# Optimization experiments

Measured on AMD Instinct MI355X. Metric: run time of the kernel, lower is better.

Reference implementation:

```python
import jax, jax.numpy as jnp
import numpy as np

N_HEAD = 16  # matches init_kwargs


def _rope_cos_sin(T, head_dim):
    # inv_freq over even indices, as in AdvancedRotaryEmbedding
    inv_freq = 1.0 / (10000.0 ** (jnp.arange(0, head_dim, 2, dtype=jnp.float32) / head_dim))
    t = jnp.arange(T, dtype=jnp.float32)
    freqs = t[:, None] * inv_freq[None, :]  # [T, head_dim/2]
    return jnp.cos(freqs), jnp.sin(freqs)


def _apply_rope(x, cos, sin):
    # x: [B, H, T, D]; cos/sin: [T, D/2] (broadcast over B, H)
    x1, x2 = x[..., 0::2], x[..., 1::2]
    # half-concat layout, faithful to the module's apply_rotary_emb
    return jnp.concatenate([x1 * cos - x2 * sin, x1 * sin + x2 * cos], axis=-1)


def reference(x, Wq, Wk, Wv, Wo):
    B, T, C = x.shape
    H = N_HEAD
    D = C // H
    # QKV projections (torch Linear: y = x @ W.T), then split heads -> [B, H, T, D]
    q = (x @ Wq.T).reshape(B, T, H, D).transpose(0, 2, 1, 3)
    k = (x @ Wk.T).reshape(B, T, H, D).transpose(0, 2, 1, 3)
    v = (x @ Wv.T).reshape(B, T, H, D).transpose(0, 2, 1, 3)
    cos, sin = _rope_cos_sin(T, D)
    cos = cos.astype(x.dtype)
    sin = sin.astype(x.dtype)
    q = _apply_rope(q, cos, sin)
    k = _apply_rope(k, cos, sin)
    # causal SDPA (eval mode -> dropout_p = 0); jax.nn expects [B, T, H, D]
    y = jax.nn.dot_product_attention(
        q.transpose(0, 2, 1, 3),
        k.transpose(0, 2, 1, 3),
        v.transpose(0, 2, 1, 3),
        is_causal=True,
    )  # [B, T, H, D]
    y = y.reshape(B, T, C)
    return y @ Wo.T


def setup_inputs() -> dict:
    key = jax.random.key(0)
    ks = jax.random.split(key, 5)
    B, T, C = 2, 2048, 1024
    s = 1.0 / np.sqrt(C)
    return {
        "x": jax.random.normal(ks[0], (B, T, C), dtype=jnp.float32),
        "Wq": jax.random.normal(ks[1], (C, C), dtype=jnp.float32) * s,
        "Wk": jax.random.normal(ks[2], (C, C), dtype=jnp.float32) * s,
        "Wv": jax.random.normal(ks[3], (C, C), dtype=jnp.float32) * s,
        "Wo": jax.random.normal(ks[4], (C, C), dtype=jnp.float32) * s,
    }
```

## Files before the change

### kernel.cpp

```cpp
#include <hip/hip_runtime.h>
#include <cstdint>
#include <cstddef>

typedef short s16x8 __attribute__((ext_vector_type(8)));
typedef float f32x4 __attribute__((ext_vector_type(4)));

#define MFMA16(a, b, c) __builtin_amdgcn_mfma_f32_16x16x32_bf16((a), (b), (c), 0, 0, 0)

constexpr int LDP = 72;
constexpr int LDW = 136;

__device__ __forceinline__ short f2bf(float f) {
    unsigned u = __builtin_bit_cast(unsigned, f);
    u += 0x7FFFu + ((u >> 16) & 1u);
    return (short)(u >> 16);
}
__device__ __forceinline__ float bf2f(short s) {
    unsigned u = ((unsigned)(unsigned short)s) << 16;
    return __builtin_bit_cast(float, u);
}
__device__ __forceinline__ unsigned pack2(float a, float b) {
    return (unsigned)(unsigned short)f2bf(a) | ((unsigned)(unsigned short)f2bf(b) << 16);
}
__device__ __forceinline__ unsigned pack2t(float a, float b) {
    unsigned ua = __builtin_bit_cast(unsigned, a);
    unsigned ub = __builtin_bit_cast(unsigned, b);
    return (ua >> 16) | (ub & 0xFFFF0000u);
}

__device__ __forceinline__ void async_ld16(const void* g, void* l) {
    __builtin_amdgcn_global_load_lds(
        (const __attribute__((address_space(1))) unsigned int*)g,
        (__attribute__((address_space(3))) unsigned int*)l, 16, 0, 0);
}

__global__ __launch_bounds__(256) void convert_kernel(
    const float* __restrict__ x, const float* __restrict__ Wq,
    const float* __restrict__ Wk, const float* __restrict__ Wv,
    const float* __restrict__ Wo, short* __restrict__ xb, short* __restrict__ wb) {
    const size_t f = ((size_t)blockIdx.x * 256 + threadIdx.x) * 8;
    const float* src;
    short* dst;
    if (f < 4194304) { src = x + f; dst = xb + f; }
    else {
        size_t wo = f - 4194304;
        int seg = (int)(wo >> 20);
        const float* ws4[4] = {Wq, Wk, Wv, Wo};
        src = ws4[seg] + (wo & 1048575u);
        dst = wb + wo;
    }
    float4 a = ((const float4*)src)[0];
    float4 b = ((const float4*)src)[1];
    *(uint4*)dst = make_uint4(pack2(a.x, a.y), pack2(a.z, a.w),
                              pack2(b.x, b.y), pack2(b.z, b.w));
}

__global__ __launch_bounds__(256) void qkv_kernel(
    const short* __restrict__ xb, const short* __restrict__ wb,
    short* __restrict__ Qo, short* __restrict__ Ko, short* __restrict__ VTo) {
    __shared__ __align__(16) short sA[128 * 64];
    __shared__ __align__(16) short sB[128 * 64];
    const int tid = threadIdx.x;
    const int w = tid >> 6, lane = tid & 63, quad = lane >> 4, l15 = lane & 15;
    const int wm = w & 1, wn = w >> 1;
    const int bx = blockIdx.x, by = blockIdx.y;
    const int m0 = by * 128;
    const int nb = bx * 128;

    f32x4 acc[4][4];
#pragma unroll
    for (int i = 0; i < 4; i++)
#pragma unroll
        for (int j = 0; j < 4; j++) acc[i][j] = f32x4{0.f, 0.f, 0.f, 0.f};

    for (int kb = 0; kb < 16; kb++) {
        const int k0 = kb * 64;
        if (kb) __syncthreads();
#pragma unroll
        for (int i = 0; i < 4; i++) {
            int c = i * 256 + tid;
            int row = c >> 3, col8 = (c & 7) * 8;
            async_ld16(xb + (size_t)(m0 + row) * 1024 + k0 + col8,
                       &sA[(i * 256 + w * 64) * 8]);
            async_ld16(wb + (size_t)(nb + row) * 1024 + k0 + col8,
                       &sB[(i * 256 + w * 64) * 8]);
        }
        __syncthreads();
#pragma unroll
        for (int ks = 0; ks < 2; ks++) {
            s16x8 av[4], bv[4];
#pragma unroll
            for (int at = 0; at < 4; at++)
                av[at] = *(const s16x8*)&sA[(wm * 64 + at * 16 + l15) * 64 + ks * 32 + quad * 8];
#pragma unroll
            for (int bt = 0; bt < 4; bt++)
                bv[bt] = *(const s16x8*)&sB[(wn * 64 + bt * 16 + l15) * 64 + ks * 32 + quad * 8];
#pragma unroll
            for (int at = 0; at < 4; at++)
#pragma unroll
                for (int bt = 0; bt < 4; bt++)
                    acc[at][bt] = MFMA16(av[at], bv[bt], acc[at][bt]);
        }
    }

    const int wsel = bx >> 3;
    const int h = (bx & 7) * 2 + wn;
    if (wsel == 2) {
#pragma unroll
        for (int at = 0; at < 4; at++) {
            int m = m0 + wm * 64 + at * 16 + quad * 4;
            int b = m >> 11, t0 = m & 2047;
            size_t base = ((size_t)((b * 16 + h) * 64)) * 2048;
#pragma unroll
            for (int bt = 0; bt < 4; bt++) {
                int d = bt * 16 + l15;
                unsigned lo = pack2(acc[at][bt][0], acc[at][bt][1]);
                unsigned hi = pack2(acc[at][bt][2], acc[at][bt][3]);
                *(uint2*)&VTo[base + (size_t)d * 2048 + t0] = make_uint2(lo, hi);
            }
        }
    } else {
        short* Out = (wsel == 0) ? Qo : Ko;
#pragma unroll
        for (int at = 0; at < 4; at++)
#pragma unroll
            for (int r = 0; r < 4; r++) {
                int m = m0 + wm * 64 + at * 16 + quad * 4 + r;
                int b = m >> 11, t = m & 2047;
                size_t base = (((size_t)(b * 16 + h)) * 2048 + t) * 64;
#pragma unroll
                for (int bt = 0; bt < 4; bt++)
                    Out[base + bt * 16 + l15] = f2bf(acc[at][bt][r]);
            }
    }
}

__global__ __launch_bounds__(256) void rope_kernel(short* __restrict__ Q, short* __restrict__ K) {
    const int rid = blockIdx.x * 256 + threadIdx.x;
    const bool isK = (rid & 65536) != 0;
    short* buf = isK ? K : Q;
    const float sc = isK ? 1.0f : 0.18033688011112042f;
    const int r2 = rid & 65535;
    const int t = r2 & 2047;
    short* row = buf + (size_t)r2 * 64;

    unsigned wv[32];
    const uint4* rp = (const uint4*)row;
#pragma unroll
    for (int c = 0; c < 8; c++) {
        uint4 v = rp[c];
        wv[c * 4 + 0] = v.x; wv[c * 4 + 1] = v.y; wv[c * 4 + 2] = v.z; wv[c * 4 + 3] = v.w;
    }
    float y1[32], y2[32];
    const float tf = (float)t;
#pragma unroll
    for (int i = 0; i < 32; i++) {
        float x1 = bf2f((short)(wv[i] & 0xFFFFu));
        float x2 = bf2f((short)(wv[i] >> 16));
        float inv = exp2f((float)i * -0.4152410118609203f);
        float rev = tf * inv * 0.15915494309189535f;
        rev = rev - floorf(rev);
        float sn = __builtin_amdgcn_sinf(rev);
        float cs = __builtin_amdgcn_cosf(rev);
        y1[i] = (x1 * cs - x2 * sn) * sc;
        y2[i] = (x1 * sn + x2 * cs) * sc;
    }
    unsigned ow[32];
#pragma unroll
    for (int i = 0; i < 16; i++) ow[i] = pack2(y1[2 * i], y1[2 * i + 1]);
#pragma unroll
    for (int i = 0; i < 16; i++) ow[16 + i] = pack2(y2[2 * i], y2[2 * i + 1]);
    uint4* wp = (uint4*)row;
#pragma unroll
    for (int c = 0; c < 8; c++)
        wp[c] = make_uint4(ow[c * 4 + 0], ow[c * 4 + 1], ow[c * 4 + 2], ow[c * 4 + 3]);
}

__global__ __launch_bounds__(256) void attn_kernel(
    const short* __restrict__ Q, const short* __restrict__ K,
    const short* __restrict__ VT, short* __restrict__ paO, float* __restrict__ ml) {
    __shared__ __align__(16) short sQP[64 * LDW];
    __shared__ __align__(16) short sK[128 * LDP];
    __shared__ __align__(16) short sVT[64 * LDW];

    const int tid = threadIdx.x;
    const int w = tid >> 6, lane = tid & 63, quad = lane >> 4, l15 = lane & 15;
    const int u = 79 - blockIdx.x;
    const int bh = blockIdx.y;

    int qt, c;
    if (u < 8)       { qt = u; c = 0; }
    else if (u < 24) { int v = u - 8;  qt = 8 + (v >> 1); c = v & 1; }
    else if (u < 48) { int v = u - 24; qt = 16 + v / 3;   c = v - 3 * (qt - 16); }
    else             { int v = u - 48; qt = 24 + (v >> 2); c = v & 3; }
    const int kbDiag = qt >> 1;
    const int kb0 = c * 4;
    const int kb1 = min(kb0 + 3, kbDiag);

    const short* Qp = Q + (size_t)bh * 2048 * 64;
    const short* Kp = K + (size_t)bh * 2048 * 64;
    const short* Vp = VT + (size_t)bh * 64 * 2048;

    const int krow = tid >> 3, kcol = (tid & 7) * 8;
    const int vrow = tid >> 4, vcol = (tid & 15) * 8;
    const short* Kld = Kp + (size_t)krow * 64 + kcol;
    const short* Vld = Vp + (size_t)vrow * 2048 + vcol;
    short* sKw = &sK[krow * LDP + kcol];
    short* sVw = &sVT[vrow * LDW + vcol];

    uint4 kr0, kr1, kr2, kr3, vr0, vr1, vr2, vr3;
#define LOADKV(KB) do {                                                  \
        const short* _kp = Kld + (size_t)(KB) * 8192;                    \
        kr0 = *(const uint4*)(_kp);                                      \
        kr1 = *(const uint4*)(_kp + 32 * 64);                            \
        kr2 = *(const uint4*)(_kp + 64 * 64);                            \
        kr3 = *(const uint4*)(_kp + 96 * 64);                            \
        const short* _vp = Vld + (KB) * 128;                             \
        vr0 = *(const uint4*)(_vp);                                      \
        vr1 = *(const uint4*)(_vp + 16 * 2048);                          \
        vr2 = *(const uint4*)(_vp + 32 * 2048);                          \
        vr3 = *(const uint4*)(_vp + 48 * 2048);                          \
    } while (0)

    s16x8 aq[2];
#pragma unroll
    for (int ks = 0; ks < 2; ks++)
        aq[ks] = *(const s16x8*)(Qp + (size_t)(qt * 64 + w * 16 + l15) * 64 + ks * 32 + quad * 8);
    LOADKV(kb0);

    f32x4 o[4];
#pragma unroll
    for (int i = 0; i < 4; i++) o[i] = f32x4{0.f, 0.f, 0.f, 0.f};
    float lrun = 0.f;
    const int q_idx = qt * 64 + w * 16 + l15;

    for (int kb = kb0; kb <= kb1; kb++) {
        __syncthreads();
        *(uint4*)(sKw)            = kr0;
        *(uint4*)(sKw + 32 * LDP) = kr1;
        *(uint4*)(sKw + 64 * LDP) = kr2;
        *(uint4*)(sKw + 96 * LDP) = kr3;
        *(uint4*)(sVw)            = vr0;
        *(uint4*)(sVw + 16 * LDW) = vr1;
        *(uint4*)(sVw + 32 * LDW) = vr2;
        *(uint4*)(sVw + 48 * LDW) = vr3;
        __syncthreads();
        if (kb < kb1) LOADKV(kb + 1);

        f32x4 sa[8];
#pragma unroll
        for (int i = 0; i < 8; i++) sa[i] = f32x4{0.f, 0.f, 0.f, 0.f};
        __builtin_amdgcn_s_setprio(1);
#pragma unroll
        for (int ks = 0; ks < 2; ks++) {
#pragma unroll
            for (int ct = 0; ct < 8; ct++) {
                s16x8 kf = *(const s16x8*)&sK[(ct * 16 + l15) * LDP + ks * 32 + quad * 8];
                sa[ct] = MFMA16(kf, aq[ks], sa[ct]);
            }
        }
        __builtin_amdgcn_s_setprio(0);

        float ps[8][4];
#pragma unroll
        for (int ct = 0; ct < 8; ct++)
#pragma unroll
            for (int r = 0; r < 4; r++) ps[ct][r] = sa[ct][r];

        if (kb == kbDiag) {
#pragma unroll
            for (int ct = 0; ct < 8; ct++) {
                int kbase = kb * 128 + ct * 16 + quad * 4;
#pragma unroll
                for (int r = 0; r < 4; r++)
                    if ((kbase + r) > q_idx) ps[ct][r] = -INFINITY;
            }
        }

        float cm[8];
#pragma unroll
        for (int ct = 0; ct < 8; ct++) {
#pragma unroll
            for (int r = 0; r < 4; r++) ps[ct][r] = __builtin_amdgcn_exp2f(ps[ct][r]);
            cm[ct] = (ps[ct][0] + ps[ct][1]) + (ps[ct][2] + ps[ct][3]);
        }
        lrun += ((cm[0] + cm[1]) + (cm[2] + cm[3])) + ((cm[4] + cm[5]) + (cm[6] + cm[7]));

#pragma unroll
        for (int ct = 0; ct < 8; ct++) {
            unsigned lo = pack2t(ps[ct][0], ps[ct][1]);
            unsigned hi = pack2t(ps[ct][2], ps[ct][3]);
            *(uint2*)&sQP[(w * 16 + l15) * LDW + ct * 16 + quad * 4] = make_uint2(lo, hi);
        }

        __builtin_amdgcn_s_setprio(1);
#pragma unroll
        for (int ks2 = 0; ks2 < 4; ks2++) {
            s16x8 pa = *(const s16x8*)&sQP[(w * 16 + l15) * LDW + ks2 * 32 + quad * 8];
#pragma unroll
            for (int ct = 0; ct < 4; ct++) {
                s16x8 vb = *(const s16x8*)&sVT[(ct * 16 + l15) * LDW + ks2 * 32 + quad * 8];
                o[ct] = MFMA16(pa, vb, o[ct]);
            }
        }
        __builtin_amdgcn_s_setprio(0);
    }
#undef LOADKV

    const size_t pbase = ((size_t)(bh * 80 + u)) * 4096;
#pragma unroll
    for (int r = 0; r < 4; r++) {
        int row = w * 16 + quad * 4 + r;
#pragma unroll
        for (int ct = 0; ct < 4; ct++)
            paO[pbase + row * 64 + ct * 16 + l15] = f2bf(o[ct][r]);
    }
    lrun += __shfl_xor(lrun, 16);
    lrun += __shfl_xor(lrun, 32);
    if (quad == 0)
        ml[(bh * 80 + u) * 64 + w * 16 + l15] = lrun;
}

__global__ __launch_bounds__(256) void combine_kernel(
    const short* __restrict__ paO, const float* __restrict__ ml, short* __restrict__ Y) {
    const int qt = blockIdx.x, bh = blockIdx.y;
    const int b = bh >> 4, h = bh & 15;
    const int nch = (qt >> 3) + 1;
    int base;
    if (qt < 8) base = qt;
    else if (qt < 16) base = 8 + 2 * (qt - 8);
    else if (qt < 24) base = 24 + 3 * (qt - 16);
    else base = 48 + 4 * (qt - 24);

    const int row = threadIdx.x >> 2;
    const int cq = (threadIdx.x & 3) * 16;

    float L = 0.f;
    for (int i = 0; i < nch; i++)
        L += ml[(bh * 80 + base + i) * 64 + row];
    const float inv = 1.0f / L;

    float acc[16];
#pragma unroll
    for (int j = 0; j < 16; j++) acc[j] = 0.f;
    for (int i = 0; i < nch; i++) {
        const short* p = paO + ((size_t)(bh * 80 + base + i)) * 4096 + row * 64 + cq;
        uint4 v0 = ((const uint4*)p)[0];
        uint4 v1 = ((const uint4*)p)[1];
        unsigned vs[8] = {v0.x, v0.y, v0.z, v0.w, v1.x, v1.y, v1.z, v1.w};
#pragma unroll
        for (int j = 0; j < 8; j++) {
            acc[2 * j + 0] += bf2f((short)(vs[j] & 0xFFFFu));
            acc[2 * j + 1] += bf2f((short)(vs[j] >> 16));
        }
    }
    const int t = qt * 64 + row;
    short* yp = Y + ((size_t)(b * 2048 + t)) * 1024 + h * 64 + cq;
    unsigned ow[8];
#pragma unroll
    for (int j = 0; j < 8; j++) ow[j] = pack2(acc[2 * j] * inv, acc[2 * j + 1] * inv);
    ((uint4*)yp)[0] = make_uint4(ow[0], ow[1], ow[2], ow[3]);
    ((uint4*)yp)[1] = make_uint4(ow[4], ow[5], ow[6], ow[7]);
}

__global__ __launch_bounds__(256) void oproj_kernel(
    const short* __restrict__ Yb, const short* __restrict__ Wob, float* __restrict__ out) {
    __shared__ __align__(16) short sA[64 * 64];
    __shared__ __align__(16) short sB[128 * 64];
    const int tid = threadIdx.x;
    const int w = tid >> 6, lane = tid & 63, quad = lane >> 4, l15 = lane & 15;
    const int m0 = blockIdx.y * 64;
    const int nb = blockIdx.x * 128;

    f32x4 acc[4][2];
#pragma unroll
    for (int i = 0; i < 4; i++)
#pragma unroll
        for (int j = 0; j < 2; j++) acc[i][j] = f32x4{0.f, 0.f, 0.f, 0.f};

    for (int kb = 0; kb < 16; kb++) {
        const int k0 = kb * 64;
        if (kb) __syncthreads();
#pragma unroll
        for (int i = 0; i < 2; i++) {
            int c = i * 256 + tid;
            int row = c >> 3, col8 = (c & 7) * 8;
            async_ld16(Yb + (size_t)(m0 + row) * 1024 + k0 + col8,
                       &sA[(i * 256 + w * 64) * 8]);
        }
#pragma unroll
        for (int i = 0; i < 4; i++) {
            int c = i * 256 + tid;
            int row = c >> 3, col8 = (c & 7) * 8;
            async_ld16(Wob + (size_t)(nb + row) * 1024 + k0 + col8,
                       &sB[(i * 256 + w * 64) * 8]);
        }
        __syncthreads();
#pragma unroll
        for (int ks = 0; ks < 2; ks++) {
            s16x8 av[4], bv[2];
#pragma unroll
            for (int at = 0; at < 4; at++)
                av[at] = *(const s16x8*)&sA[(at * 16 + l15) * 64 + ks * 32 + quad * 8];
#pragma unroll
            for (int bt = 0; bt < 2; bt++)
                bv[bt] = *(const s16x8*)&sB[(w * 32 + bt * 16 + l15) * 64 + ks * 32 + quad * 8];
#pragma unroll
            for (int at = 0; at < 4; at++)
#pragma unroll
                for (int bt = 0; bt < 2; bt++)
                    acc[at][bt] = MFMA16(av[at], bv[bt], acc[at][bt]);
        }
    }
#pragma unroll
    for (int at = 0; at < 4; at++)
#pragma unroll
        for (int r = 0; r < 4; r++) {
            int m = m0 + at * 16 + quad * 4 + r;
#pragma unroll
            for (int bt = 0; bt < 2; bt++) {
                int n = nb + w * 32 + bt * 16 + l15;
                out[(size_t)m * 1024 + n] = acc[at][bt][r];
            }
        }
}

extern "C" void kernel_launch(void* const* d_in, const int* in_sizes, int n_in,
                              void* d_out, int out_size, void* d_ws, size_t ws_size,
                              hipStream_t stream) {
    (void)in_sizes; (void)n_in; (void)out_size; (void)ws_size;
    const float* x  = (const float*)d_in[0];
    const float* Wq = (const float*)d_in[1];
    const float* Wk = (const float*)d_in[2];
    const float* Wv = (const float*)d_in[3];
    const float* Wo = (const float*)d_in[4];
    float* out = (float*)d_out;

    const size_t NE = (size_t)2 * 16 * 2048 * 64;
    short* Q   = (short*)d_ws;
    short* K   = Q + NE;
    short* VT  = K + NE;
    short* Y   = VT + NE;
    short* xb  = Y;
    short* wb  = Y + NE;
    short* paO = wb + NE;
    float* ml  = (float*)(paO + (size_t)32 * 80 * 4096);

    convert_kernel<<<4096, 256, 0, stream>>>(x, Wq, Wk, Wv, Wo, xb, wb);
    qkv_kernel<<<dim3(24, 32), 256, 0, stream>>>(xb, wb, Q, K, VT);
    rope_kernel<<<512, 256, 0, stream>>>(Q, K);
    attn_kernel<<<dim3(80, 32), 256, 0, stream>>>(Q, K, VT, paO, ml);
    combine_kernel<<<dim3(32, 32), 256, 0, stream>>>(paO, ml, Y);
    oproj_kernel<<<dim3(8, 64), 256, 0, stream>>>(Y, wb + 3 * 1048576, out);
}
```

Baseline: 197.2 us.

## Load V fragments directly from global memory, drop V shared tile

Removes the shared-memory staging of the transposed V tile: each wave now loads its PV MFMA B-fragments directly from global memory into registers, double-buffered across the four k-steps and prefetching the next block's first step. This cuts LDS traffic and shared memory footprint, and the launch bound now requests 4 blocks per CU to exploit the smaller LDS use. In exchange every wave redundantly fetches the same V data from global/L2, and global load latency now sits inside the PV loop. Register pressure rises under the tighter occupancy bound.

```diff
diff --git a/kernel.cpp b/kernel.cpp
--- a/kernel.cpp
+++ b/kernel.cpp
@@ -176,12 +176,11 @@
         wp[c] = make_uint4(ow[c * 4 + 0], ow[c * 4 + 1], ow[c * 4 + 2], ow[c * 4 + 3]);
 }
 
-__global__ __launch_bounds__(256) void attn_kernel(
+__global__ __launch_bounds__(256, 4) void attn_kernel(
     const short* __restrict__ Q, const short* __restrict__ K,
     const short* __restrict__ VT, short* __restrict__ paO, float* __restrict__ ml) {
     __shared__ __align__(16) short sQP[64 * LDW];
     __shared__ __align__(16) short sK[128 * LDP];
-    __shared__ __align__(16) short sVT[64 * LDW];
 
     const int tid = threadIdx.x;
     const int w = tid >> 6, lane = tid & 63, quad = lane >> 4, l15 = lane & 15;
@@ -202,31 +201,31 @@
     const short* Vp = VT + (size_t)bh * 64 * 2048;
 
     const int krow = tid >> 3, kcol = (tid & 7) * 8;
-    const int vrow = tid >> 4, vcol = (tid & 15) * 8;
     const short* Kld = Kp + (size_t)krow * 64 + kcol;
-    const short* Vld = Vp + (size_t)vrow * 2048 + vcol;
     short* sKw = &sK[krow * LDP + kcol];
-    short* sVw = &sVT[vrow * LDW + vcol];
-
-    uint4 kr0, kr1, kr2, kr3, vr0, vr1, vr2, vr3;
-#define LOADKV(KB) do {                                                  \
+
+    uint4 kr0, kr1, kr2, kr3;
+#define LOADK(KB) do {                                                   \
         const short* _kp = Kld + (size_t)(KB) * 8192;                    \
         kr0 = *(const uint4*)(_kp);                                      \
         kr1 = *(const uint4*)(_kp + 32 * 64);                            \
         kr2 = *(const uint4*)(_kp + 64 * 64);                            \
         kr3 = *(const uint4*)(_kp + 96 * 64);                            \
-        const short* _vp = Vld + (KB) * 128;                             \
-        vr0 = *(const uint4*)(_vp);                                      \
-        vr1 = *(const uint4*)(_vp + 16 * 2048);                          \
-        vr2 = *(const uint4*)(_vp + 32 * 2048);                          \
-        vr3 = *(const uint4*)(_vp + 48 * 2048);                          \
     } while (0)
+
+    const short* Vf = Vp + (size_t)l15 * 2048 + quad * 8;
+#define VFRAG(CT, KB, KS2) \
+    (*(const s16x8*)(Vf + (size_t)(CT) * 32768 + (KB) * 128 + (KS2) * 32))
 
     s16x8 aq[2];
 #pragma unroll
     for (int ks = 0; ks < 2; ks++)
         aq[ks] = *(const s16x8*)(Qp + (size_t)(qt * 64 + w * 16 + l15) * 64 + ks * 32 + quad * 8);
-    LOADKV(kb0);
+    LOADK(kb0);
+
+    s16x8 va0 = VFRAG(0, kb0, 0), va1 = VFRAG(1, kb0, 0),
+          va2 = VFRAG(2, kb0, 0), va3 = VFRAG(3, kb0, 0);
+    s16x8 vb0, vb1, vb2, vb3;
 
     f32x4 o[4];
 #pragma unroll
@@ -240,12 +239,8 @@
         *(uint4*)(sKw + 32 * LDP) = kr1;
         *(uint4*)(sKw + 64 * LDP) = kr2;
         *(uint4*)(sKw + 96 * LDP) = kr3;
-        *(uint4*)(sVw)            = vr0;
-        *(uint4*)(sVw + 16 * LDW) = vr1;
-        *(uint4*)(sVw + 32 * LDW) = vr2;
-        *(uint4*)(sVw + 48 * LDW) = vr3;
         __syncthreads();
-        if (kb < kb1) LOADKV(kb + 1);
+        if (kb < kb1) LOADK(kb + 1);
 
         f32x4 sa[8];
 #pragma unroll
@@ -294,18 +289,35 @@
         }
 
         __builtin_amdgcn_s_setprio(1);
-#pragma unroll
-        for (int ks2 = 0; ks2 < 4; ks2++) {
-            s16x8 pa = *(const s16x8*)&sQP[(w * 16 + l15) * LDW + ks2 * 32 + quad * 8];
-#pragma unroll
-            for (int ct = 0; ct < 4; ct++) {
-                s16x8 vb = *(const s16x8*)&sVT[(ct * 16 + l15) * LDW + ks2 * 32 + quad * 8];
-                o[ct] = MFMA16(pa, vb, o[ct]);
-            }
+        {
+            s16x8 pa;
+            vb0 = VFRAG(0, kb, 1); vb1 = VFRAG(1, kb, 1);
+            vb2 = VFRAG(2, kb, 1); vb3 = VFRAG(3, kb, 1);
+            pa = *(const s16x8*)&sQP[(w * 16 + l15) * LDW + 0 * 32 + quad * 8];
+            o[0] = MFMA16(pa, va0, o[0]); o[1] = MFMA16(pa, va1, o[1]);
+            o[2] = MFMA16(pa, va2, o[2]); o[3] = MFMA16(pa, va3, o[3]);
+            va0 = VFRAG(0, kb, 2); va1 = VFRAG(1, kb, 2);
+            va2 = VFRAG(2, kb, 2); va3 = VFRAG(3, kb, 2);
+            pa = *(const s16x8*)&sQP[(w * 16 + l15) * LDW + 1 * 32 + quad * 8];
+            o[0] = MFMA16(pa, vb0, o[0]); o[1] = MFMA16(pa, vb1, o[1]);
+            o[2] = MFMA16(pa, vb2, o[2]); o[3] = MFMA16(pa, vb3, o[3]);
+            vb0 = VFRAG(0, kb, 3); vb1 = VFRAG(1, kb, 3);
+            vb2 = VFRAG(2, kb, 3); vb3 = VFRAG(3, kb, 3);
+            pa = *(const s16x8*)&sQP[(w * 16 + l15) * LDW + 2 * 32 + quad * 8];
+            o[0] = MFMA16(pa, va0, o[0]); o[1] = MFMA16(pa, va1, o[1]);
+            o[2] = MFMA16(pa, va2, o[2]); o[3] = MFMA16(pa, va3, o[3]);
+            if (kb < kb1) {
+                va0 = VFRAG(0, kb + 1, 0); va1 = VFRAG(1, kb + 1, 0);
+                va2 = VFRAG(2, kb + 1, 0); va3 = VFRAG(3, kb + 1, 0);
+            }
+            pa = *(const s16x8*)&sQP[(w * 16 + l15) * LDW + 3 * 32 + quad * 8];
+            o[0] = MFMA16(pa, vb0, o[0]); o[1] = MFMA16(pa, vb1, o[1]);
+            o[2] = MFMA16(pa, vb2, o[2]); o[3] = MFMA16(pa, vb3, o[3]);
         }
         __builtin_amdgcn_s_setprio(0);
     }
-#undef LOADKV
+#undef LOADK
+#undef VFRAG
 
     const size_t pbase = ((size_t)(bh * 80 + u)) * 4096;
 #pragma unroll
```

After: 256.5 us. 1.3x slower.
